# Optimization experiments

Hardware: AMD Instinct MI355X
Metric: run time of the kernel (lower is better)

## Reference

```python
import jax, jax.numpy as jnp
import numpy as np

DIM = 256; K = 3; PAD = 1; DIL = 1; B = 16; H = 56; W = 56
SP = 8           # share_planes
RADIX = 2
ATTN = max(DIM * RADIX // 4, 32)   # 128
EMB = K * K * DIM // SP            # 288

def conv(x, w, pad=0, dil=1, groups=1):
    return jax.lax.conv_general_dilated(
        x, w, (1, 1), [(pad, pad), (pad, pad)], rhs_dilation=(dil, dil),
        feature_group_count=groups, dimension_numbers=('NCHW', 'OIHW', 'NCHW'))

def bn(x, g, b, m, v, eps=1e-5):
    # eval-mode BatchNorm2d
    s = g * jax.lax.rsqrt(v + eps)
    return x * s[None, :, None, None] + (b - m * s)[None, :, None, None]

def gn(x, g, b, groups, eps=1e-5):
    Bb, C, Hh, Ww = x.shape
    xg = x.reshape(Bb, groups, C // groups, Hh, Ww)
    mu = xg.mean((2, 3, 4), keepdims=True)
    var = xg.var((2, 3, 4), keepdims=True)
    xg = (xg - mu) * jax.lax.rsqrt(var + eps)
    return xg.reshape(Bb, C, Hh, Ww) * g[None, :, None, None] + b[None, :, None, None]

def unfold3(x):
    # im2col for 3x3, stride 1, pad 1 -> (B, C, K*K, H, W)
    Bb, C, Hh, Ww = x.shape
    p = (K - 1) // 2
    xp = jnp.pad(x, ((0, 0), (0, 0), (p, p), (p, p)))
    return jnp.stack([xp[:, :, i:i + Hh, j:j + Ww] for i in range(K) for j in range(K)], axis=2)

def reference(x, ke_w, ke_g, ke_b, ke_m, ke_v, e1_w, e1_g, e1_b, e1_m, e1_v,
              e2_w, e2_b, gng, gnb, c1_w, c1_g, c1_b, c1_m, c1_v,
              b2_g, b2_b, b2_m, b2_v, s1_w, s1_b, s1_g, s1_bb, s1_m, s1_v,
              s2_w, s2_b):
    Bb = x.shape[0]
    # key embed: grouped kxk conv + BN + ReLU
    k = jax.nn.relu(bn(conv(x, ke_w, pad=PAD, dil=DIL, groups=4), ke_g, ke_b, ke_m, ke_v))
    qk = jnp.concatenate([x, k], axis=1)                     # (B, 2*DIM, H, W)
    # dynamic kernel branch
    wemb = jax.nn.relu(bn(conv(qk, e1_w), e1_g, e1_b, e1_m, e1_v))
    wemb = conv(wemb, e2_w) + e2_b[None, :, None, None]
    wemb = gn(wemb, gng, gnb, DIM // SP)                     # GroupNorm(dim//8 groups)
    wemb = wemb.reshape(Bb, DIM // SP, K * K, H, W)
    # value branch
    xq = bn(conv(x, c1_w), c1_g, c1_b, c1_m, c1_v)
    # local dynamic convolution: per-pixel kernel shared across SP channels
    patches = unfold3(xq).reshape(Bb, DIM // SP, SP, K * K, H, W)
    y = (patches * wemb[:, :, None]).sum(3).reshape(Bb, DIM, H, W)
    y = bn(y, b2_g, b2_b, b2_m, b2_v)
    y = y * jax.nn.sigmoid(y)                                # swish
    # split attention over radix=2 branches (y, k)
    xs = jnp.stack([y, k], axis=2)                           # (B, C, 2, H, W)
    gap = xs.sum(2).mean((2, 3), keepdims=True)              # (B, C, 1, 1)
    a = jax.nn.relu(bn(conv(gap, s1_w) + s1_b[None, :, None, None], s1_g, s1_bb, s1_m, s1_v))
    a = conv(a, s2_w) + s2_b[None, :, None, None]            # (B, 2*C, 1, 1)
    a = jax.nn.softmax(a.reshape(Bb, DIM, RADIX), axis=2)
    out = (xs * a[:, :, :, None, None]).sum(2)
    return out

def setup_inputs():
    key = jax.random.key(0)
    ks = iter(jax.random.split(key, 40))
    def n(shape, s=1.0):
        return jax.random.normal(next(ks), shape, jnp.float32) * s
    def u(shape):
        return jax.random.uniform(next(ks), shape, jnp.float32, minval=0.5, maxval=1.5)
    d = {}
    d['x'] = n((B, DIM, H, W))
    d['ke_w'] = n((DIM, DIM // 4, K, K), 0.05)
    d['ke_g'] = u((DIM,)); d['ke_b'] = n((DIM,), 0.1); d['ke_m'] = n((DIM,), 0.1); d['ke_v'] = u((DIM,))
    d['e1_w'] = n((DIM // 2, 2 * DIM, 1, 1), 0.05)
    d['e1_g'] = u((DIM // 2,)); d['e1_b'] = n((DIM // 2,), 0.1); d['e1_m'] = n((DIM // 2,), 0.1); d['e1_v'] = u((DIM // 2,))
    d['e2_w'] = n((EMB, DIM // 2, 1, 1), 0.05); d['e2_b'] = n((EMB,), 0.1)
    d['gng'] = u((EMB,)); d['gnb'] = n((EMB,), 0.1)
    d['c1_w'] = n((DIM, DIM, 1, 1), 0.05)
    d['c1_g'] = u((DIM,)); d['c1_b'] = n((DIM,), 0.1); d['c1_m'] = n((DIM,), 0.1); d['c1_v'] = u((DIM,))
    d['b2_g'] = u((DIM,)); d['b2_b'] = n((DIM,), 0.1); d['b2_m'] = n((DIM,), 0.1); d['b2_v'] = u((DIM,))
    d['s1_w'] = n((ATTN, DIM, 1, 1), 0.05); d['s1_b'] = n((ATTN,), 0.1)
    d['s1_g'] = u((ATTN,)); d['s1_bb'] = n((ATTN,), 0.1); d['s1_m'] = n((ATTN,), 0.1); d['s1_v'] = u((ATTN,))
    d['s2_w'] = n((RADIX * DIM, ATTN, 1, 1), 0.05); d['s2_b'] = n((RADIX * DIM,), 0.1)
    return d
```

## Files before the change

kernel.cpp:

```cpp
#include <hip/hip_runtime.h>
#include <hip/hip_bf16.h>

typedef __hip_bfloat16 bf16;
typedef float f32x4 __attribute__((ext_vector_type(4)));
typedef short s16x8 __attribute__((ext_vector_type(8)));

#define NPIX 3136
#define HDIM 56
#define CDIM 256

static __device__ __forceinline__ float b2f(bf16 v){ return __bfloat162float(v); }
static __device__ __forceinline__ bf16  f2b(float v){ return __float2bfloat16(v); }

#define O_KE_S 0
#define O_KE_B 256
#define O_E1_S 512
#define O_E1_B 640
#define O_C1_S 768
#define O_C1_B 1024
#define O_B2_S 1280
#define O_B2_B 1536
#define O_S1_S 1792
#define O_S1_B 1920
#define O_E2B  2048
#define O_GNS  2336
#define O_GAP  3360
#define O_ATT  7456

__global__ void prep(
    const float* __restrict__ kew, const float* __restrict__ e1w,
    const float* __restrict__ e2w, const float* __restrict__ c1w,
    const float* keg, const float* keb, const float* kem, const float* kev,
    const float* e1g, const float* e1b, const float* e1m, const float* e1v,
    const float* e2b,
    const float* c1g, const float* c1b, const float* c1m, const float* c1v,
    const float* b2g, const float* b2b, const float* b2m, const float* b2v,
    const float* s1g, const float* s1bb, const float* s1m, const float* s1v,
    bf16* kewT, bf16* e1wb, bf16* e2wb, bf16* c1wb, float* o)
{
    int bid = blockIdx.x, t = threadIdx.x;
    if (bid < 576) {
        int i = bid * 256 + t;
        int ci = i & 63, co_l = (i >> 6) & 63;
        int gt = i >> 12;
        int tap = gt % 9, g = gt / 9;
        int co = g * 64 + co_l;
        kewT[i] = f2b(kew[(co * 64 + ci) * 9 + tap]);
    } else if (bid < 832) {
        int i = (bid - 576) * 256 + t; e1wb[i] = f2b(e1w[i]);
    } else if (bid < 976) {
        int i = (bid - 832) * 256 + t; e2wb[i] = f2b(e2w[i]);
    } else if (bid < 1232) {
        int i = (bid - 976) * 256 + t; c1wb[i] = f2b(c1w[i]);
    } else if (bid == 1232) {
        const float eps = 1e-5f;
        {
            float s = keg[t] * rsqrtf(kev[t] + eps);
            o[O_KE_S + t] = s; o[O_KE_B + t] = keb[t] - kem[t] * s;
            s = c1g[t] * rsqrtf(c1v[t] + eps);
            o[O_C1_S + t] = s; o[O_C1_B + t] = c1b[t] - c1m[t] * s;
            s = b2g[t] * rsqrtf(b2v[t] + eps);
            o[O_B2_S + t] = s; o[O_B2_B + t] = b2b[t] - b2m[t] * s;
        }
        if (t < 128) {
            float s = e1g[t] * rsqrtf(e1v[t] + eps);
            o[O_E1_S + t] = s; o[O_E1_B + t] = e1b[t] - e1m[t] * s;
            s = s1g[t] * rsqrtf(s1v[t] + eps);
            o[O_S1_S + t] = s; o[O_S1_B + t] = s1bb[t] - s1m[t] * s;
        }
        for (int i = t; i < 288; i += 256) o[O_E2B + i] = e2b[i];
    } else {
        int j = (bid - 1233) * 256 + t;
        if (j < 1024) o[O_GNS + j] = 0.f;
        else          o[O_GAP + j - 1024] = 0.f;
    }
}

__global__ __launch_bounds__(256) void cvt_x(const float* __restrict__ x, bf16* __restrict__ xh)
{
    int b = blockIdx.y;
    int p0 = blockIdx.x * 64;
    __shared__ bf16 T[64][264];
    int t = threadIdx.x;
    for (int it = 0; it < 16; it++) {
        int slot = t + it * 256;
        int c = slot >> 4, ch4 = slot & 15;
        float4 v = *(const float4*)(x + ((long)b * CDIM + c) * NPIX + p0 + ch4 * 4);
        T[ch4 * 4 + 0][c] = f2b(v.x);
        T[ch4 * 4 + 1][c] = f2b(v.y);
        T[ch4 * 4 + 2][c] = f2b(v.z);
        T[ch4 * 4 + 3][c] = f2b(v.w);
    }
    __syncthreads();
    for (int it = 0; it < 8; it++) {
        int slot = t + it * 256;
        int p = slot >> 5, cc = slot & 31;
        *(float4*)(xh + ((long)b * NPIX + p0 + p) * CDIM + cc * 8) = *(const float4*)&T[p][cc * 8];
    }
}

__global__ __launch_bounds__(256) void gconv_mfma(
    const bf16* __restrict__ xh, const bf16* __restrict__ wT,
    const float* __restrict__ scale, const float* __restrict__ bias,
    bf16* __restrict__ kh)
{
    int b = blockIdx.z, g = blockIdx.y;
    int p0 = blockIdx.x * 64;
    __shared__ bf16 As[5 * 58 * 72];
    int t = threadIdx.x;
    int wv = t >> 6, lane = t & 63, q = lane >> 4, ln = lane & 15;
    int r_first = p0 / HDIM - 1;

    #pragma unroll
    for (int i = 0; i < 10; i++) {
        int slot = t + i * 256;
        if (slot < 2320) {
            int chunk = slot & 7, pos = slot >> 3;
            int ri = pos / 58, ci = pos - ri * 58;
            int h = r_first + ri, w = ci - 1;
            float4 v = {0.f, 0.f, 0.f, 0.f};
            if ((unsigned)h < HDIM && (unsigned)w < HDIM)
                v = *(const float4*)(xh + ((long)b * NPIX + h * HDIM + w) * CDIM + g * 64 + chunk * 8);
            *(float4*)&As[pos * 72 + chunk * 8] = v;
        }
    }
    __syncthreads();

    int posp[4];
    #pragma unroll
    for (int pt = 0; pt < 4; pt++) {
        int p = p0 + pt * 16 + ln;
        int hp = p / HDIM, wp = p - hp * HDIM;
        posp[pt] = (hp - r_first) * 58 + wp + 1;
    }
    const bf16* wbase = wT + ((long)(g * 9) * 64 + wv * 16 + ln) * 64;

    f32x4 acc[4] = {};
    #pragma unroll
    for (int tap = 0; tap < 9; tap++) {
        int dpos = (tap / 3 - 1) * 58 + (tap % 3 - 1);
        const bf16* wp = wbase + tap * 64 * 64;
        s16x8 B0 = *(const s16x8*)(wp + q * 8);
        s16x8 B1 = *(const s16x8*)(wp + 32 + q * 8);
        #pragma unroll
        for (int pt = 0; pt < 4; pt++) {
            int base = (posp[pt] + dpos) * 72 + q * 8;
            s16x8 a0 = *(const s16x8*)&As[base];
            s16x8 a1 = *(const s16x8*)&As[base + 32];
            acc[pt] = __builtin_amdgcn_mfma_f32_16x16x32_bf16(a0, B0, acc[pt], 0, 0, 0);
            acc[pt] = __builtin_amdgcn_mfma_f32_16x16x32_bf16(a1, B1, acc[pt], 0, 0, 0);
        }
    }

    __syncthreads();
    int co = g * 64 + wv * 16 + ln;
    float sc = scale[co], bi = bias[co];
    #pragma unroll
    for (int pt = 0; pt < 4; pt++)
        #pragma unroll
        for (int r = 0; r < 4; r++)
            As[(pt * 16 + q * 4 + r) * 72 + wv * 16 + ln] = f2b(fmaxf(acc[pt][r] * sc + bi, 0.f));
    __syncthreads();
    #pragma unroll
    for (int i = 0; i < 2; i++) {
        int slot = t + i * 256;
        int row = slot >> 3, cc = slot & 7;
        *(float4*)(kh + ((long)b * NPIX + p0 + row) * CDIM + g * 64 + cc * 8) = *(const float4*)&As[row * 72 + cc * 8];
    }
}

template<int MODE>
__global__ __launch_bounds__(256) void mfma_gemm(
    const bf16* __restrict__ Wt, const bf16* __restrict__ X0, const bf16* __restrict__ X1,
    int C0, int K, int M,
    const float* __restrict__ scale, const float* __restrict__ bias,
    bf16* __restrict__ Y, float* __restrict__ gnsum)
{
    int b = blockIdx.z;
    int p0 = blockIdx.x * 64;
    int m0 = blockIdx.y * 128;
    __shared__ bf16 SH[64 * 72 + 128 * 72];
    bf16* As = SH;
    bf16* Bs = SH + 64 * 72;
    __shared__ float gs[64];
    int t = threadIdx.x;
    int wv = t >> 6, lane = t & 63, q = lane >> 4, ln = lane & 15;
    if (MODE == 1) { if (t < 64) gs[t] = 0.f; }

    f32x4 acc[4][2] = {};
    for (int k0 = 0; k0 < K; k0 += 64) {
        __syncthreads();
        #pragma unroll
        for (int i = 0; i < 2; i++) {
            int slot = t + i * 256;
            int chunk = slot & 7, row = slot >> 3;
            int ch = k0 + chunk * 8;
            const bf16* src = (ch < C0)
                ? X0 + ((long)b * NPIX + p0 + row) * C0 + ch
                : X1 + ((long)b * NPIX + p0 + row) * (K - C0) + (ch - C0);
            *(float4*)&As[row * 72 + chunk * 8] = *(const float4*)src;
        }
        #pragma unroll
        for (int i = 0; i < 4; i++) {
            int slot = t + i * 256;
            int chunk = slot & 7, row = slot >> 3;
            int m = m0 + row;
            float4 v = {0.f, 0.f, 0.f, 0.f};
            if (m < M) v = *(const float4*)(Wt + (long)m * K + k0 + chunk * 8);
            *(float4*)&Bs[row * 72 + chunk * 8] = v;
        }
        __syncthreads();
        #pragma unroll
        for (int kk = 0; kk < 2; kk++) {
            s16x8 a[4];
            #pragma unroll
            for (int pt = 0; pt < 4; pt++)
                a[pt] = *(const s16x8*)&As[(pt * 16 + ln) * 72 + kk * 32 + q * 8];
            #pragma unroll
            for (int mi = 0; mi < 2; mi++) {
                s16x8 bb = *(const s16x8*)&Bs[(wv * 32 + mi * 16 + ln) * 72 + kk * 32 + q * 8];
                #pragma unroll
                for (int pt = 0; pt < 4; pt++)
                    acc[pt][mi] = __builtin_amdgcn_mfma_f32_16x16x32_bf16(a[pt], bb, acc[pt][mi], 0, 0, 0);
            }
        }
    }

    __syncthreads();
    bf16* T = SH;
    #pragma unroll
    for (int mi = 0; mi < 2; mi++) {
        int m = m0 + wv * 32 + mi * 16 + ln;
        int mc = (m > M - 1) ? (M - 1) : m;
        float sc = 1.f, bi;
        if (MODE == 0 || MODE == 2) { sc = scale[mc]; bi = bias[mc]; }
        else bi = bias[mc];
        float ps = 0.f, pq = 0.f;
        #pragma unroll
        for (int pt = 0; pt < 4; pt++) {
            #pragma unroll
            for (int r = 0; r < 4; r++) {
                float v = acc[pt][mi][r] * sc + bi;
                if (MODE == 0) v = fmaxf(v, 0.f);
                if (MODE == 1) { ps += v; pq += v * v; }
                T[(pt * 16 + q * 4 + r) * 144 + wv * 32 + mi * 16 + ln] = f2b(v);
            }
        }
        if (MODE == 1 && m < M) {
            int grp = m / 9;
            atomicAdd(&gs[grp * 2], ps);
            atomicAdd(&gs[grp * 2 + 1], pq);
        }
    }
    __syncthreads();
    #pragma unroll
    for (int i = 0; i < 4; i++) {
        int slot = t + i * 256;
        int chunk = slot & 15, row = slot >> 4;
        int m = m0 + chunk * 8;
        if (m + 8 <= M)
            *(float4*)(Y + ((long)b * NPIX + p0 + row) * M + m) = *(const float4*)&T[row * 144 + chunk * 8];
    }
    if (MODE == 1 && t < 64) atomicAdd(&gnsum[b * 64 + t], gs[t]);
}

__global__ __launch_bounds__(256) void dynconv(
    const bf16* __restrict__ xq, const bf16* __restrict__ wemb,
    const float* __restrict__ gnsum,
    const float* __restrict__ gng, const float* __restrict__ gnb,
    const float* __restrict__ b2s, const float* __restrict__ b2b,
    bf16* __restrict__ y)
{
    int id = blockIdx.x * 256 + threadIdx.x;
    int grp = id & 31;
    int p = (id >> 5) % NPIX;
    int b = id / (NPIX * 32);
    int h = p / HDIM, w = p % HDIM;
    float S = gnsum[b * 64 + grp * 2], Q = gnsum[b * 64 + grp * 2 + 1];
    float mu = S * (1.f / 28224.f);
    float var = Q * (1.f / 28224.f) - mu * mu;
    float rs = rsqrtf(fmaxf(var, 0.f) + 1e-5f);
    const bf16* wp = wemb + ((long)b * NPIX + p) * 288 + grp * 9;
    float wv[9];
    #pragma unroll
    for (int tp = 0; tp < 9; tp++)
        wv[tp] = (b2f(wp[tp]) - mu) * rs * gng[grp * 9 + tp] + gnb[grp * 9 + tp];
    float acc[8] = {};
    #pragma unroll
    for (int tp = 0; tp < 9; tp++) {
        int h2 = h + tp / 3 - 1, w2 = w + tp % 3 - 1;
        if ((unsigned)h2 >= HDIM || (unsigned)w2 >= HDIM) continue;
        const bf16* xp = xq + ((long)b * NPIX + h2 * HDIM + w2) * CDIM + grp * 8;
        s16x8 xv = *(const s16x8*)xp;
        const bf16* xb = (const bf16*)&xv;
        float wt = wv[tp];
        #pragma unroll
        for (int i = 0; i < 8; i++) acc[i] += b2f(xb[i]) * wt;
    }
    bf16 outv[8];
    #pragma unroll
    for (int i = 0; i < 8; i++) {
        int c = grp * 8 + i;
        float v = acc[i] * b2s[c] + b2b[c];
        outv[i] = f2b(v / (1.f + __expf(-v)));
    }
    *(float4*)(y + ((long)b * NPIX + p) * CDIM + grp * 8) = *(const float4*)outv;
}

__global__ void gapk(const bf16* __restrict__ y, const bf16* __restrict__ k, float* __restrict__ gap)
{
    int b = blockIdx.x, chunk = blockIdx.y, c = threadIdx.x;
    float s = 0.f;
    for (int i = 0; i < 64; i++) {
        long off = ((long)b * NPIX + chunk * 64 + i) * CDIM + c;
        s += b2f(y[off]) + b2f(k[off]);
    }
    atomicAdd(&gap[b * 256 + c], s * (1.f / NPIX));
}

__global__ void attnk(const float* __restrict__ gap,
                      const float* __restrict__ s1w, const float* __restrict__ s1b,
                      const float* __restrict__ s1s, const float* __restrict__ s1bi,
                      const float* __restrict__ s2w, const float* __restrict__ s2b,
                      float* __restrict__ att)
{
    int b = blockIdx.x, t = threadIdx.x;
    __shared__ float g[256], a1[128];
    for (int i = t; i < 256; i += 128) g[i] = gap[b * 256 + i];
    __syncthreads();
    float s = 0.f;
    for (int ci = 0; ci < 256; ci++) s += s1w[t * 256 + ci] * g[ci];
    s += s1b[t];
    s = s * s1s[t] + s1bi[t];
    a1[t] = fmaxf(s, 0.f);
    __syncthreads();
    for (int c = t; c < 256; c += 128) {
        float v0 = s2b[2 * c], v1 = s2b[2 * c + 1];
        for (int ci = 0; ci < 128; ci++) {
            float av = a1[ci];
            v0 += s2w[(2 * c) * 128 + ci] * av;
            v1 += s2w[(2 * c + 1) * 128 + ci] * av;
        }
        float m = fmaxf(v0, v1);
        float e0 = __expf(v0 - m), e1 = __expf(v1 - m);
        float inv = 1.f / (e0 + e1);
        att[(b * 256 + c) * 2 + 0] = e0 * inv;
        att[(b * 256 + c) * 2 + 1] = e1 * inv;
    }
}

__global__ __launch_bounds__(256) void finalk(
    const bf16* __restrict__ y, const bf16* __restrict__ k,
    const float* __restrict__ att, float* __restrict__ out)
{
    int b = blockIdx.z, c0 = blockIdx.y * 64, p0 = blockIdx.x * 64;
    __shared__ bf16 Ys[64][72], Ks[64][72];
    int t = threadIdx.x;
    #pragma unroll
    for (int i = 0; i < 2; i++) {
        int slot = t + i * 256;
        int row = slot >> 3, cc = slot & 7;
        long off = ((long)b * NPIX + p0 + row) * CDIM + c0 + cc * 8;
        *(float4*)&Ys[row][cc * 8] = *(const float4*)(y + off);
        *(float4*)&Ks[row][cc * 8] = *(const float4*)(k + off);
    }
    __syncthreads();
    int c_l = t >> 2, pc = t & 3;
    int c = c0 + c_l;
    float a0 = att[(b * 256 + c) * 2], a1 = att[(b * 256 + c) * 2 + 1];
    float4 o[4];
    float* of = (float*)o;
    #pragma unroll
    for (int j = 0; j < 16; j++) {
        int p = pc * 16 + j;
        of[j] = b2f(Ys[p][c_l]) * a0 + b2f(Ks[p][c_l]) * a1;
    }
    float* dst = out + ((long)b * CDIM + c) * NPIX + p0 + pc * 16;
    #pragma unroll
    for (int j = 0; j < 4; j++) ((float4*)dst)[j] = o[j];
}

extern "C" void kernel_launch(void* const* d_in, const int* in_sizes, int n_in,
                              void* d_out, int out_size, void* d_ws, size_t ws_size,
                              hipStream_t stream)
{
    const float* x    = (const float*)d_in[0];
    const float* ke_w = (const float*)d_in[1];
    const float* ke_g = (const float*)d_in[2];
    const float* ke_b = (const float*)d_in[3];
    const float* ke_m = (const float*)d_in[4];
    const float* ke_v = (const float*)d_in[5];
    const float* e1_w = (const float*)d_in[6];
    const float* e1_g = (const float*)d_in[7];
    const float* e1_b = (const float*)d_in[8];
    const float* e1_m = (const float*)d_in[9];
    const float* e1_v = (const float*)d_in[10];
    const float* e2_w = (const float*)d_in[11];
    const float* e2_b = (const float*)d_in[12];
    const float* gng  = (const float*)d_in[13];
    const float* gnb  = (const float*)d_in[14];
    const float* c1_w = (const float*)d_in[15];
    const float* c1_g = (const float*)d_in[16];
    const float* c1_b = (const float*)d_in[17];
    const float* c1_m = (const float*)d_in[18];
    const float* c1_v = (const float*)d_in[19];
    const float* b2_g = (const float*)d_in[20];
    const float* b2_b = (const float*)d_in[21];
    const float* b2_m = (const float*)d_in[22];
    const float* b2_v = (const float*)d_in[23];
    const float* s1_w = (const float*)d_in[24];
    const float* s1_b = (const float*)d_in[25];
    const float* s1_g = (const float*)d_in[26];
    const float* s1_bb= (const float*)d_in[27];
    const float* s1_m = (const float*)d_in[28];
    const float* s1_v = (const float*)d_in[29];
    const float* s2_w = (const float*)d_in[30];
    const float* s2_b = (const float*)d_in[31];

    float* fold = (float*)d_ws;
    bf16* wsb   = (bf16*)((char*)d_ws + 65536);
    bf16* xh   = wsb;
    bf16* kh   = xh + 12845056L;
    bf16* wemb = kh + 12845056L;
    bf16* w1   = wemb + 14450688L;
    bf16* xq   = w1;
    bf16* yb   = xh;
    bf16* kewT = w1 + 12845056L;
    bf16* e1wb = kewT + 147456L;
    bf16* e2wb = e1wb + 65536L;
    bf16* c1wb = e2wb + 36864L;

    prep<<<dim3(1253), dim3(256), 0, stream>>>(
        ke_w, e1_w, e2_w, c1_w,
        ke_g, ke_b, ke_m, ke_v, e1_g, e1_b, e1_m, e1_v, e2_b,
        c1_g, c1_b, c1_m, c1_v, b2_g, b2_b, b2_m, b2_v,
        s1_g, s1_bb, s1_m, s1_v,
        kewT, e1wb, e2wb, c1wb, fold);

    cvt_x<<<dim3(49, 16), dim3(256), 0, stream>>>(x, xh);

    gconv_mfma<<<dim3(49, 4, 16), dim3(256), 0, stream>>>(
        xh, kewT, fold + O_KE_S, fold + O_KE_B, kh);

    mfma_gemm<0><<<dim3(49, 1, 16), dim3(256), 0, stream>>>(
        e1wb, xh, kh, 256, 512, 128, fold + O_E1_S, fold + O_E1_B, w1, nullptr);

    mfma_gemm<1><<<dim3(49, 3, 16), dim3(256), 0, stream>>>(
        e2wb, w1, (const bf16*)nullptr, 128, 128, 288, (const float*)nullptr, fold + O_E2B,
        wemb, fold + O_GNS);

    mfma_gemm<2><<<dim3(49, 2, 16), dim3(256), 0, stream>>>(
        c1wb, xh, (const bf16*)nullptr, 256, 256, 256, fold + O_C1_S, fold + O_C1_B, xq, nullptr);

    dynconv<<<dim3(6272), dim3(256), 0, stream>>>(
        xq, wemb, fold + O_GNS, gng, gnb,
        fold + O_B2_S, fold + O_B2_B, yb);

    gapk<<<dim3(16, 49), dim3(256), 0, stream>>>(yb, kh, fold + O_GAP);

    attnk<<<dim3(16), dim3(128), 0, stream>>>(
        fold + O_GAP, s1_w, s1_b, fold + O_S1_S, fold + O_S1_B, s2_w, s2_b, fold + O_ATT);

    finalk<<<dim3(49, 4, 16), dim3(256), 0, stream>>>(yb, kh, fold + O_ATT, (float*)d_out);
}
```

Measured before the change: 367.5 us.

## Store input in zero-padded layout, read conv taps from global, vectorize GAP

The bf16 copy of x is now written into a 58x58 spatially padded layout, and cvt_x zeroes the border. This lets the grouped 3x3 conv load its taps straight from global memory with no bounds checks. Before, each block staged a 5-row halo tile (290 positions for 64 output pixels) into shared memory, and that staging step is removed. The two 1x1 GEMMs that read x are changed to index the padded layout. The global-average-pool kernel now uses 16-byte vector loads plus a shared-memory reduction instead of scalar loads. The risk is that each input element is re-fetched up to nine times through the caches rather than served from LDS.

```diff
diff --git a/kernel.cpp b/kernel.cpp
--- a/kernel.cpp
+++ b/kernel.cpp
@@ -8,6 +8,7 @@
 #define NPIX 3136
 #define HDIM 56
 #define CDIM 256
+#define PPIX 3364
 
 static __device__ __forceinline__ float b2f(bf16 v){ return __bfloat162float(v); }
 static __device__ __forceinline__ bf16  f2b(float v){ return __float2bfloat16(v); }
@@ -82,6 +83,20 @@
     int p0 = blockIdx.x * 64;
     __shared__ bf16 T[64][264];
     int t = threadIdx.x;
+
+    if (blockIdx.x == 0) {
+        float4 z = {0.f, 0.f, 0.f, 0.f};
+        for (int s = t; s < 7296; s += 256) {
+            int pi = s >> 5, cc = s & 31;
+            int pos;
+            if (pi < 58)       pos = pi;
+            else if (pi < 116) pos = 57 * 58 + (pi - 58);
+            else if (pi < 172) pos = (pi - 115) * 58;
+            else               pos = (pi - 171) * 58 + 57;
+            *(float4*)(xh + ((long)b * PPIX + pos) * 256 + cc * 8) = z;
+        }
+    }
+
     for (int it = 0; it < 16; it++) {
         int slot = t + it * 256;
         int c = slot >> 4, ch4 = slot & 15;
@@ -95,81 +110,69 @@
     for (int it = 0; it < 8; it++) {
         int slot = t + it * 256;
         int p = slot >> 5, cc = slot & 31;
-        *(float4*)(xh + ((long)b * NPIX + p0 + p) * CDIM + cc * 8) = *(const float4*)&T[p][cc * 8];
+        int pl = p0 + p;
+        int h = pl / HDIM, w = pl - h * HDIM;
+        *(float4*)(xh + ((long)b * PPIX + (h + 1) * 58 + (w + 1)) * 256 + cc * 8) = *(const float4*)&T[p][cc * 8];
     }
 }
 
 __global__ __launch_bounds__(256) void gconv_mfma(
-    const bf16* __restrict__ xh, const bf16* __restrict__ wT,
+    const bf16* __restrict__ xp, const bf16* __restrict__ wT,
     const float* __restrict__ scale, const float* __restrict__ bias,
     bf16* __restrict__ kh)
 {
     int b = blockIdx.z, g = blockIdx.y;
     int p0 = blockIdx.x * 64;
-    __shared__ bf16 As[5 * 58 * 72];
+    __shared__ bf16 T[64 * 72];
     int t = threadIdx.x;
     int wv = t >> 6, lane = t & 63, q = lane >> 4, ln = lane & 15;
-    int r_first = p0 / HDIM - 1;
-
-    #pragma unroll
-    for (int i = 0; i < 10; i++) {
-        int slot = t + i * 256;
-        if (slot < 2320) {
-            int chunk = slot & 7, pos = slot >> 3;
-            int ri = pos / 58, ci = pos - ri * 58;
-            int h = r_first + ri, w = ci - 1;
-            float4 v = {0.f, 0.f, 0.f, 0.f};
-            if ((unsigned)h < HDIM && (unsigned)w < HDIM)
-                v = *(const float4*)(xh + ((long)b * NPIX + h * HDIM + w) * CDIM + g * 64 + chunk * 8);
-            *(float4*)&As[pos * 72 + chunk * 8] = v;
-        }
-    }
-    __syncthreads();
-
-    int posp[4];
+
+    const bf16* rp[4][3];
     #pragma unroll
     for (int pt = 0; pt < 4; pt++) {
         int p = p0 + pt * 16 + ln;
         int hp = p / HDIM, wp = p - hp * HDIM;
-        posp[pt] = (hp - r_first) * 58 + wp + 1;
+        long base = ((long)b * PPIX + (hp + 1) * 58 + (wp + 1)) * 256 + g * 64 + q * 8;
+        rp[pt][0] = xp + base - 58 * 256;
+        rp[pt][1] = xp + base;
+        rp[pt][2] = xp + base + 58 * 256;
     }
     const bf16* wbase = wT + ((long)(g * 9) * 64 + wv * 16 + ln) * 64;
 
     f32x4 acc[4] = {};
     #pragma unroll
     for (int tap = 0; tap < 9; tap++) {
-        int dpos = (tap / 3 - 1) * 58 + (tap % 3 - 1);
-        const bf16* wp = wbase + tap * 64 * 64;
-        s16x8 B0 = *(const s16x8*)(wp + q * 8);
-        s16x8 B1 = *(const s16x8*)(wp + 32 + q * 8);
+        int dr = tap / 3;
+        int dc = tap % 3 - 1;
+        const bf16* wq = wbase + tap * 64 * 64;
+        s16x8 B0 = *(const s16x8*)(wq + q * 8);
+        s16x8 B1 = *(const s16x8*)(wq + 32 + q * 8);
         #pragma unroll
         for (int pt = 0; pt < 4; pt++) {
-            int base = (posp[pt] + dpos) * 72 + q * 8;
-            s16x8 a0 = *(const s16x8*)&As[base];
-            s16x8 a1 = *(const s16x8*)&As[base + 32];
+            s16x8 a0 = *(const s16x8*)(rp[pt][dr] + dc * 256);
+            s16x8 a1 = *(const s16x8*)(rp[pt][dr] + dc * 256 + 32);
             acc[pt] = __builtin_amdgcn_mfma_f32_16x16x32_bf16(a0, B0, acc[pt], 0, 0, 0);
             acc[pt] = __builtin_amdgcn_mfma_f32_16x16x32_bf16(a1, B1, acc[pt], 0, 0, 0);
         }
     }
 
-    __syncthreads();
     int co = g * 64 + wv * 16 + ln;
     float sc = scale[co], bi = bias[co];
     #pragma unroll
     for (int pt = 0; pt < 4; pt++)
         #pragma unroll
         for (int r = 0; r < 4; r++)
-            As[(pt * 16 + q * 4 + r) * 72 + wv * 16 + ln] = f2b(fmaxf(acc[pt][r] * sc + bi, 0.f));
+            T[(pt * 16 + q * 4 + r) * 72 + wv * 16 + ln] = f2b(fmaxf(acc[pt][r] * sc + bi, 0.f));
     __syncthreads();
     #pragma unroll
     for (int i = 0; i < 2; i++) {
         int slot = t + i * 256;
         int row = slot >> 3, cc = slot & 7;
-        *(float4*)(kh + ((long)b * NPIX + p0 + row) * CDIM + g * 64 + cc * 8) = *(const float4*)&As[row * 72 + cc * 8];
-    }
-}
-
-template<int MODE>
+        *(float4*)(kh + ((long)b * NPIX + p0 + row) * CDIM + g * 64 + cc * 8) = *(const float4*)&T[row * 72 + cc * 8];
+    }
+}
+
+template<int MODE, int PADX0>
 __global__ __launch_bounds__(256) void mfma_gemm(
     const bf16* __restrict__ Wt, const bf16* __restrict__ X0, const bf16* __restrict__ X1,
     int C0, int K, int M,
@@ -195,9 +198,15 @@
             int slot = t + i * 256;
             int chunk = slot & 7, row = slot >> 3;
             int ch = k0 + chunk * 8;
-            const bf16* src = (ch < C0)
-                ? X0 + ((long)b * NPIX + p0 + row) * C0 + ch
-                : X1 + ((long)b * NPIX + p0 + row) * (K - C0) + (ch - C0);
+            const bf16* src;
+            if (ch < C0) {
+                long pp = p0 + row;
+                long pidx = PADX0 ? ((long)b * PPIX + pp + 2 * (pp / HDIM) + 59)
+                                  : ((long)b * NPIX + pp);
+                src = X0 + pidx * C0 + ch;
+            } else {
+                src = X1 + ((long)b * NPIX + p0 + row) * (K - C0) + (ch - C0);
+            }
             *(float4*)&As[row * 72 + chunk * 8] = *(const float4*)src;
         }
         #pragma unroll
@@ -307,15 +316,30 @@
     *(float4*)(y + ((long)b * NPIX + p) * CDIM + grp * 8) = *(const float4*)outv;
 }
 
-__global__ void gapk(const bf16* __restrict__ y, const bf16* __restrict__ k, float* __restrict__ gap)
-{
-    int b = blockIdx.x, chunk = blockIdx.y, c = threadIdx.x;
+__global__ __launch_bounds__(256) void gapk(const bf16* __restrict__ y, const bf16* __restrict__ k, float* __restrict__ gap)
+{
+    int b = blockIdx.x, chunk = blockIdx.y;
+    int t = threadIdx.x;
+    int cc = t & 31, pl = t >> 5;
+    float acc[8] = {};
+    #pragma unroll
+    for (int i = 0; i < 8; i++) {
+        long off = ((long)b * NPIX + chunk * 64 + pl * 8 + i) * CDIM + cc * 8;
+        s16x8 yv = *(const s16x8*)(y + off);
+        s16x8 kv = *(const s16x8*)(k + off);
+        const bf16* ya = (const bf16*)&yv;
+        const bf16* ka = (const bf16*)&kv;
+        #pragma unroll
+        for (int j = 0; j < 8; j++) acc[j] += b2f(ya[j]) + b2f(ka[j]);
+    }
+    __shared__ float R[8][256];
+    #pragma unroll
+    for (int j = 0; j < 8; j++) R[pl][cc * 8 + j] = acc[j];
+    __syncthreads();
     float s = 0.f;
-    for (int i = 0; i < 64; i++) {
-        long off = ((long)b * NPIX + chunk * 64 + i) * CDIM + c;
-        s += b2f(y[off]) + b2f(k[off]);
-    }
-    atomicAdd(&gap[b * 256 + c], s * (1.f / NPIX));
+    #pragma unroll
+    for (int p = 0; p < 8; p++) s += R[p][t];
+    atomicAdd(&gap[b * 256 + t], s * (1.f / NPIX));
 }
 
 __global__ void attnk(const float* __restrict__ gap,
@@ -420,7 +444,7 @@
     float* fold = (float*)d_ws;
     bf16* wsb   = (bf16*)((char*)d_ws + 65536);
     bf16* xh   = wsb;
-    bf16* kh   = xh + 12845056L;
+    bf16* kh   = xh + 13778944L;
     bf16* wemb = kh + 12845056L;
     bf16* w1   = wemb + 14450688L;
     bf16* xq   = w1;
@@ -442,14 +466,14 @@
     gconv_mfma<<<dim3(49, 4, 16), dim3(256), 0, stream>>>(
         xh, kewT, fold + O_KE_S, fold + O_KE_B, kh);
 
-    mfma_gemm<0><<<dim3(49, 1, 16), dim3(256), 0, stream>>>(
+    mfma_gemm<0, 1><<<dim3(49, 1, 16), dim3(256), 0, stream>>>(
         e1wb, xh, kh, 256, 512, 128, fold + O_E1_S, fold + O_E1_B, w1, nullptr);
 
-    mfma_gemm<1><<<dim3(49, 3, 16), dim3(256), 0, stream>>>(
+    mfma_gemm<1, 0><<<dim3(49, 3, 16), dim3(256), 0, stream>>>(
         e2wb, w1, (const bf16*)nullptr, 128, 128, 288, (const float*)nullptr, fold + O_E2B,
         wemb, fold + O_GNS);
 
-    mfma_gemm<2><<<dim3(49, 2, 16), dim3(256), 0, stream>>>(
+    mfma_gemm<2, 1><<<dim3(49, 2, 16), dim3(256), 0, stream>>>(
         c1wb, xh, (const bf16*)nullptr, 256, 256, 256, fold + O_C1_S, fold + O_C1_B, xq, nullptr);
 
     dynconv<<<dim3(6272), dim3(256), 0, stream>>>(
```

Measured after the change: 447.6 us. +21.8%, slower.
